# Kernel optimization log

Hardware: AMD Instinct MI355X
Metric: run time of the kernel (lower is better)

Reference implementation:

```python
import jax, jax.numpy as jnp
import numpy as np

B, S, D, UNITS = 8, 2048, 1024, 1024

def setup_inputs() -> dict:
    key = jax.random.key(0)
    k1, k2, k3, k4 = jax.random.split(key, 4)
    scale = 1.0 / np.sqrt(D)
    return {
        "inputs": jax.random.normal(k1, (B, S, D), dtype=jnp.float32),
        "Wq": jax.random.normal(k2, (D, UNITS), dtype=jnp.float32) * scale,
        "Wk": jax.random.normal(k3, (D, UNITS), dtype=jnp.float32) * scale,
        "Wv": jax.random.normal(k4, (D, UNITS), dtype=jnp.float32) * scale,
    }

def reference(inputs, Wq, Wk, Wv):
    # QKV projections (bias-free Dense): [B,S,D] @ [D,U] -> [B,S,U]
    q = jnp.einsum("bsd,du->bsu", inputs, Wq)
    k = jnp.einsum("bsd,du->bsu", inputs, Wk)
    v = jnp.einsum("bsd,du->bsu", inputs, Wv)
    # scaled dot-product scores [B,S,S]
    scores = jnp.einsum("bqu,bku->bqk", q, k) / jnp.sqrt(jnp.float32(UNITS))
    attn = jax.nn.softmax(scores, axis=-1)
    # weighted sum of values [B,S,U]
    return jnp.einsum("bqk,bku->bqu", attn, v)
```

## Files before the change

kernel.cpp:

```cpp
#include <hip/hip_runtime.h>


#define BM 128
#define BN 128
#define BK 64

typedef _Float16 half8  __attribute__((ext_vector_type(8)));
typedef float    floatx4 __attribute__((ext_vector_type(4)));

__device__ __forceinline__ void stage_async(const _Float16* __restrict__ src, int ld,
                                            _Float16* __restrict__ dst, int wave, int lane) {
#pragma unroll
    for (int i = 0; i < 4; ++i) {
        int chunk = i * 4 + wave;
        int L = chunk * 64 + lane;
        int row = L >> 3, c8 = L & 7;
        int cg = c8 ^ (row & 7);
        __builtin_amdgcn_global_load_lds(
            (const __attribute__((address_space(1))) unsigned int*)(src + (size_t)row * ld + cg * 8),
            (__attribute__((address_space(3))) unsigned int*)(dst + chunk * 512),
            16, 0, 0);
    }
}

__device__ __forceinline__ void mfma_accum(const _Float16* __restrict__ As,
                                           const _Float16* __restrict__ Bs,
                                           int wm, int wn, int l15, int q4,
                                           floatx4 acc[4][4]) {
#pragma unroll
    for (int kk = 0; kk < 2; ++kk) {
        half8 a[4], b[4];
#pragma unroll
        for (int i = 0; i < 4; ++i) {
            int row = wm * 64 + i * 16 + l15;
            int cg = (kk * 4 + q4) ^ (row & 7);
            a[i] = *(const half8*)(As + row * 64 + cg * 8);
        }
#pragma unroll
        for (int j = 0; j < 4; ++j) {
            int row = wn * 64 + j * 16 + l15;
            int cg = (kk * 4 + q4) ^ (row & 7);
            b[j] = *(const half8*)(Bs + row * 64 + cg * 8);
        }
#pragma unroll
        for (int i = 0; i < 4; ++i)
#pragma unroll
            for (int j = 0; j < 4; ++j)
                acc[i][j] = __builtin_amdgcn_mfma_f32_16x16x32_f16(a[i], b[j], acc[i][j], 0, 0, 0);
    }
}

__global__ void cast_x(const float* __restrict__ X, _Float16* __restrict__ Xh) {
    size_t i = ((size_t)blockIdx.x * 256 + threadIdx.x) * 8;
    float4 v0 = *(const float4*)(X + i);
    float4 v1 = *(const float4*)(X + i + 4);
    half8 h;
    h[0] = (_Float16)v0.x; h[1] = (_Float16)v0.y; h[2] = (_Float16)v0.z; h[3] = (_Float16)v0.w;
    h[4] = (_Float16)v1.x; h[5] = (_Float16)v1.y; h[6] = (_Float16)v1.z; h[7] = (_Float16)v1.w;
    *(half8*)(Xh + i) = h;
}

__global__ void prep_weights(const float* __restrict__ Wq, const float* __restrict__ Wk,
                             const float* __restrict__ Wv, _Float16* __restrict__ WbT,
                             float* __restrict__ rowsum) {
    int g = blockIdx.z;
    const float* W = (g == 0) ? Wq : (g == 1) ? Wk : Wv;
    __shared__ float tile[32][33];
    int u0 = blockIdx.x * 32, d0 = blockIdx.y * 32;
    int tx = threadIdx.x & 31, ty = threadIdx.x >> 5;
#pragma unroll
    for (int i = 0; i < 32; i += 8)
        tile[ty + i][tx] = W[(size_t)(d0 + ty + i) * 1024 + (u0 + tx)];
    __syncthreads();
#pragma unroll
    for (int i = 0; i < 32; i += 8)
        WbT[(size_t)g * 1024 * 1024 + (size_t)(u0 + ty + i) * 1024 + (d0 + tx)] =
            (_Float16)tile[tx][ty + i];
    int gid = (blockIdx.z * gridDim.y + blockIdx.y) * gridDim.x + blockIdx.x;
    int tg = gid * 256 + threadIdx.x;
    if (tg < 8 * 2048) rowsum[tg] = 0.0f;
}

__global__ void qkv_gemm(const _Float16* __restrict__ Xh, const _Float16* __restrict__ WbT,
                         _Float16* __restrict__ Qh, _Float16* __restrict__ Kh,
                         _Float16* __restrict__ Vt) {
    __shared__ __align__(16) _Float16 As[BM * BK];
    __shared__ __align__(16) _Float16 Bs[BN * BK];
    int t = threadIdx.x;
    int lane = t & 63, wave = t >> 6;
    int wm = wave >> 1, wn = wave & 1;
    int l15 = lane & 15, q4 = lane >> 4;
    int m0 = blockIdx.y * BM, n0 = blockIdx.x * BN;
    floatx4 acc[4][4] = {};
    for (int kt = 0; kt < 1024; kt += BK) {
        __syncthreads();
        stage_async(Xh + (size_t)m0 * 1024 + kt, 1024, As, wave, lane);
        stage_async(WbT + (size_t)n0 * 1024 + kt, 1024, Bs, wave, lane);
        __syncthreads();
        mfma_accum(As, Bs, wm, wn, l15, q4, acc);
    }
#pragma unroll
    for (int i = 0; i < 4; ++i)
#pragma unroll
        for (int j = 0; j < 4; ++j)
#pragma unroll
            for (int r = 0; r < 4; ++r) {
                int m = m0 + wm * 64 + i * 16 + q4 * 4 + r;
                int n = n0 + wn * 64 + j * 16 + l15;
                int which = n >> 10, u = n & 1023;
                int b = m >> 11, s = m & 2047;
                _Float16 val = (_Float16)acc[i][j][r];
                if (which == 0)      Qh[((size_t)b * 2048 + s) * 1024 + u] = val;
                else if (which == 1) Kh[((size_t)b * 2048 + s) * 1024 + u] = val;
                else                 Vt[((size_t)b * 1024 + u) * 2048 + s] = val;
            }
}

__global__ void scores_gemm(const _Float16* __restrict__ Qh, const _Float16* __restrict__ Kh,
                            _Float16* __restrict__ P, float* __restrict__ rowsum) {
    __shared__ __align__(16) _Float16 As[BM * BK];
    __shared__ __align__(16) _Float16 Bs[BN * BK];
    int t = threadIdx.x;
    int lane = t & 63, wave = t >> 6;
    int wm = wave >> 1, wn = wave & 1;
    int l15 = lane & 15, q4 = lane >> 4;
    int m0 = blockIdx.y * BM, n0 = blockIdx.x * BN;
    int batch = blockIdx.z;
    const _Float16* A = Qh + (size_t)batch * 2048 * 1024;
    const _Float16* B = Kh + (size_t)batch * 2048 * 1024;
    floatx4 acc[4][4] = {};
    for (int kt = 0; kt < 1024; kt += BK) {
        __syncthreads();
        stage_async(A + (size_t)m0 * 1024 + kt, 1024, As, wave, lane);
        stage_async(B + (size_t)n0 * 1024 + kt, 1024, Bs, wave, lane);
        __syncthreads();
        mfma_accum(As, Bs, wm, wn, l15, q4, acc);
    }
    _Float16* Pb = P + (size_t)batch * 2048 * 2048;
    float* rs = rowsum + batch * 2048;
#pragma unroll
    for (int i = 0; i < 4; ++i)
#pragma unroll
        for (int r = 0; r < 4; ++r) {
            int m = m0 + wm * 64 + i * 16 + q4 * 4 + r;
            float sum = 0.0f;
#pragma unroll
            for (int j = 0; j < 4; ++j) {
                int n = n0 + wn * 64 + j * 16 + l15;
                float e = __expf(acc[i][j][r] * 0.03125f);
                Pb[(size_t)m * 2048 + n] = (_Float16)e;
                sum += e;
            }
            sum += __shfl_xor(sum, 1);
            sum += __shfl_xor(sum, 2);
            sum += __shfl_xor(sum, 4);
            sum += __shfl_xor(sum, 8);
            if (l15 == 0) atomicAdd(&rs[m], sum);
        }
}

__global__ void pv_gemm(const _Float16* __restrict__ P, const _Float16* __restrict__ Vt,
                        const float* __restrict__ rowsum, float* __restrict__ out) {
    __shared__ __align__(16) _Float16 As[BM * BK];
    __shared__ __align__(16) _Float16 Bs[BN * BK];
    int t = threadIdx.x;
    int lane = t & 63, wave = t >> 6;
    int wm = wave >> 1, wn = wave & 1;
    int l15 = lane & 15, q4 = lane >> 4;
    int m0 = blockIdx.y * BM, n0 = blockIdx.x * BN;
    int batch = blockIdx.z;
    const _Float16* A = P + (size_t)batch * 2048 * 2048;
    const _Float16* B = Vt + (size_t)batch * 1024 * 2048;
    floatx4 acc[4][4] = {};
    for (int kt = 0; kt < 2048; kt += BK) {
        __syncthreads();
        stage_async(A + (size_t)m0 * 2048 + kt, 2048, As, wave, lane);
        stage_async(B + (size_t)n0 * 2048 + kt, 2048, Bs, wave, lane);
        __syncthreads();
        mfma_accum(As, Bs, wm, wn, l15, q4, acc);
    }
    const float* rs = rowsum + batch * 2048;
    float* ob = out + (size_t)batch * 2048 * 1024;
#pragma unroll
    for (int i = 0; i < 4; ++i)
#pragma unroll
        for (int r = 0; r < 4; ++r) {
            int m = m0 + wm * 64 + i * 16 + q4 * 4 + r;
            float inv = 1.0f / rs[m];
#pragma unroll
            for (int j = 0; j < 4; ++j) {
                int n = n0 + wn * 64 + j * 16 + l15;
                ob[(size_t)m * 1024 + n] = acc[i][j][r] * inv;
            }
        }
}

extern "C" void kernel_launch(void* const* d_in, const int* in_sizes, int n_in,
                              void* d_out, int out_size, void* d_ws, size_t ws_size,
                              hipStream_t stream) {
    const float* X  = (const float*)d_in[0];
    const float* Wq = (const float*)d_in[1];
    const float* Wk = (const float*)d_in[2];
    const float* Wv = (const float*)d_in[3];
    float* out = (float*)d_out;

    char* ws = (char*)d_ws;
    size_t off = 0;
    _Float16* Xh  = (_Float16*)(ws + off); off += (size_t)8 * 2048 * 1024 * 2;
    _Float16* WbT = (_Float16*)(ws + off); off += (size_t)3 * 1024 * 1024 * 2;
    _Float16* Qh  = (_Float16*)(ws + off); off += (size_t)8 * 2048 * 1024 * 2;
    _Float16* Kh  = (_Float16*)(ws + off); off += (size_t)8 * 2048 * 1024 * 2;
    _Float16* Vt  = (_Float16*)(ws + off); off += (size_t)8 * 1024 * 2048 * 2;
    _Float16* P   = (_Float16*)(ws + off); off += (size_t)8 * 2048 * 2048 * 2;
    float* rowsum = (float*)(ws + off);    off += (size_t)8 * 2048 * 4;

    cast_x     <<<dim3(8192, 1, 1), 256, 0, stream>>>(X, Xh);
    prep_weights<<<dim3(32, 32, 3), 256, 0, stream>>>(Wq, Wk, Wv, WbT, rowsum);
    qkv_gemm   <<<dim3(24, 128, 1), 256, 0, stream>>>(Xh, WbT, Qh, Kh, Vt);
    scores_gemm<<<dim3(16, 16, 8),  256, 0, stream>>>(Qh, Kh, P, rowsum);
    pv_gemm    <<<dim3(8, 16, 8),   256, 0, stream>>>(P, Vt, rowsum, out);
}
```

Baseline: 428.9 us.

## Switch to 32x32x16 MFMA and compute softmax row sums inside PV GEMM

Replaces the 16x16x32 MFMA tiling with 32x32x16 MFMA fragments in all three GEMMs, halving LDS fragment loads per FLOP. Removes the atomic row-sum accumulation from the scores epilogue and the zero-init in weight prep. Instead, pv_gemm sums the fp16 P values it already loads from LDS and normalizes with a lane shuffle. This trades global atomics for extra fp16 adds in the PV inner loop, and the sums now come from fp16-rounded P with half-precision partial adds, which may slightly change accuracy.

```diff
diff --git a/kernel.cpp b/kernel.cpp
--- a/kernel.cpp
+++ b/kernel.cpp
@@ -5,8 +5,9 @@
 #define BN 128
 #define BK 64
 
-typedef _Float16 half8  __attribute__((ext_vector_type(8)));
-typedef float    floatx4 __attribute__((ext_vector_type(4)));
+typedef _Float16 half8   __attribute__((ext_vector_type(8)));
+typedef _Float16 half2v  __attribute__((ext_vector_type(2)));
+typedef float    floatx16 __attribute__((ext_vector_type(16)));
 
 __device__ __forceinline__ void stage_async(const _Float16* __restrict__ src, int ld,
                                             _Float16* __restrict__ dst, int wave, int lane) {
@@ -25,44 +26,50 @@
 
 __device__ __forceinline__ void mfma_accum(const _Float16* __restrict__ As,
                                            const _Float16* __restrict__ Bs,
-                                           int wm, int wn, int l15, int q4,
-                                           floatx4 acc[4][4]) {
-#pragma unroll
-    for (int kk = 0; kk < 2; ++kk) {
-        half8 a[4], b[4];
-#pragma unroll
-        for (int i = 0; i < 4; ++i) {
-            int row = wm * 64 + i * 16 + l15;
-            int cg = (kk * 4 + q4) ^ (row & 7);
-            a[i] = *(const half8*)(As + row * 64 + cg * 8);
-        }
-#pragma unroll
-        for (int j = 0; j < 4; ++j) {
-            int row = wn * 64 + j * 16 + l15;
-            int cg = (kk * 4 + q4) ^ (row & 7);
-            b[j] = *(const half8*)(Bs + row * 64 + cg * 8);
-        }
-#pragma unroll
-        for (int i = 0; i < 4; ++i)
-#pragma unroll
-            for (int j = 0; j < 4; ++j)
-                acc[i][j] = __builtin_amdgcn_mfma_f32_16x16x32_f16(a[i], b[j], acc[i][j], 0, 0, 0);
-    }
+                                           int wm, int wn, int l31, int h,
+                                           floatx16 acc[2][2]) {
+#pragma unroll
+    for (int kc = 0; kc < 4; ++kc) {
+        int kh = kc * 2 + h;
+        half8 a[2], b[2];
+#pragma unroll
+        for (int fi = 0; fi < 2; ++fi) {
+            int row = wm * 64 + fi * 32 + l31;
+            a[fi] = *(const half8*)(As + row * 64 + (kh ^ (row & 7)) * 8);
+        }
+#pragma unroll
+        for (int fj = 0; fj < 2; ++fj) {
+            int row = wn * 64 + fj * 32 + l31;
+            b[fj] = *(const half8*)(Bs + row * 64 + (kh ^ (row & 7)) * 8);
+        }
+#pragma unroll
+        for (int fi = 0; fi < 2; ++fi)
+#pragma unroll
+            for (int fj = 0; fj < 2; ++fj)
+                acc[fi][fj] = __builtin_amdgcn_mfma_f32_32x32x16_f16(a[fi], b[fj], acc[fi][fj], 0, 0, 0);
+    }
+}
+
+__device__ __forceinline__ float sum8h(half8 a) {
+    union { half8 v; half2v h2[4]; } u; u.v = a;
+    half2v s0 = u.h2[0] + u.h2[1];
+    half2v s1 = u.h2[2] + u.h2[3];
+    half2v s  = s0 + s1;
+    return (float)s[0] + (float)s[1];
 }
 
 __global__ void cast_x(const float* __restrict__ X, _Float16* __restrict__ Xh) {
     size_t i = ((size_t)blockIdx.x * 256 + threadIdx.x) * 8;
     float4 v0 = *(const float4*)(X + i);
     float4 v1 = *(const float4*)(X + i + 4);
-    half8 h;
-    h[0] = (_Float16)v0.x; h[1] = (_Float16)v0.y; h[2] = (_Float16)v0.z; h[3] = (_Float16)v0.w;
-    h[4] = (_Float16)v1.x; h[5] = (_Float16)v1.y; h[6] = (_Float16)v1.z; h[7] = (_Float16)v1.w;
-    *(half8*)(Xh + i) = h;
+    half8 hh;
+    hh[0] = (_Float16)v0.x; hh[1] = (_Float16)v0.y; hh[2] = (_Float16)v0.z; hh[3] = (_Float16)v0.w;
+    hh[4] = (_Float16)v1.x; hh[5] = (_Float16)v1.y; hh[6] = (_Float16)v1.z; hh[7] = (_Float16)v1.w;
+    *(half8*)(Xh + i) = hh;
 }
 
 __global__ void prep_weights(const float* __restrict__ Wq, const float* __restrict__ Wk,
-                             const float* __restrict__ Wv, _Float16* __restrict__ WbT,
-                             float* __restrict__ rowsum) {
+                             const float* __restrict__ Wv, _Float16* __restrict__ WbT) {
     int g = blockIdx.z;
     const float* W = (g == 0) ? Wq : (g == 1) ? Wk : Wv;
     __shared__ float tile[32][33];
@@ -76,9 +83,6 @@
     for (int i = 0; i < 32; i += 8)
         WbT[(size_t)g * 1024 * 1024 + (size_t)(u0 + ty + i) * 1024 + (d0 + tx)] =
             (_Float16)tile[tx][ty + i];
-    int gid = (blockIdx.z * gridDim.y + blockIdx.y) * gridDim.x + blockIdx.x;
-    int tg = gid * 256 + threadIdx.x;
-    if (tg < 8 * 2048) rowsum[tg] = 0.0f;
 }
 
 __global__ void qkv_gemm(const _Float16* __restrict__ Xh, const _Float16* __restrict__ WbT,
@@ -89,27 +93,27 @@
     int t = threadIdx.x;
     int lane = t & 63, wave = t >> 6;
     int wm = wave >> 1, wn = wave & 1;
-    int l15 = lane & 15, q4 = lane >> 4;
+    int l31 = lane & 31, h = lane >> 5;
     int m0 = blockIdx.y * BM, n0 = blockIdx.x * BN;
-    floatx4 acc[4][4] = {};
+    floatx16 acc[2][2] = {};
     for (int kt = 0; kt < 1024; kt += BK) {
         __syncthreads();
         stage_async(Xh + (size_t)m0 * 1024 + kt, 1024, As, wave, lane);
         stage_async(WbT + (size_t)n0 * 1024 + kt, 1024, Bs, wave, lane);
         __syncthreads();
-        mfma_accum(As, Bs, wm, wn, l15, q4, acc);
-    }
-#pragma unroll
-    for (int i = 0; i < 4; ++i)
-#pragma unroll
-        for (int j = 0; j < 4; ++j)
-#pragma unroll
-            for (int r = 0; r < 4; ++r) {
-                int m = m0 + wm * 64 + i * 16 + q4 * 4 + r;
-                int n = n0 + wn * 64 + j * 16 + l15;
+        mfma_accum(As, Bs, wm, wn, l31, h, acc);
+    }
+#pragma unroll
+    for (int fi = 0; fi < 2; ++fi)
+#pragma unroll
+        for (int fj = 0; fj < 2; ++fj)
+#pragma unroll
+            for (int r = 0; r < 16; ++r) {
+                int m = m0 + wm * 64 + fi * 32 + (r & 3) + 8 * (r >> 2) + 4 * h;
+                int n = n0 + wn * 64 + fj * 32 + l31;
                 int which = n >> 10, u = n & 1023;
                 int b = m >> 11, s = m & 2047;
-                _Float16 val = (_Float16)acc[i][j][r];
+                _Float16 val = (_Float16)acc[fi][fj][r];
                 if (which == 0)      Qh[((size_t)b * 2048 + s) * 1024 + u] = val;
                 else if (which == 1) Kh[((size_t)b * 2048 + s) * 1024 + u] = val;
                 else                 Vt[((size_t)b * 1024 + u) * 2048 + s] = val;
@@ -117,80 +121,95 @@
 }
 
 __global__ void scores_gemm(const _Float16* __restrict__ Qh, const _Float16* __restrict__ Kh,
-                            _Float16* __restrict__ P, float* __restrict__ rowsum) {
+                            _Float16* __restrict__ P) {
     __shared__ __align__(16) _Float16 As[BM * BK];
     __shared__ __align__(16) _Float16 Bs[BN * BK];
     int t = threadIdx.x;
     int lane = t & 63, wave = t >> 6;
     int wm = wave >> 1, wn = wave & 1;
-    int l15 = lane & 15, q4 = lane >> 4;
+    int l31 = lane & 31, h = lane >> 5;
     int m0 = blockIdx.y * BM, n0 = blockIdx.x * BN;
     int batch = blockIdx.z;
     const _Float16* A = Qh + (size_t)batch * 2048 * 1024;
     const _Float16* B = Kh + (size_t)batch * 2048 * 1024;
-    floatx4 acc[4][4] = {};
+    floatx16 acc[2][2] = {};
     for (int kt = 0; kt < 1024; kt += BK) {
         __syncthreads();
         stage_async(A + (size_t)m0 * 1024 + kt, 1024, As, wave, lane);
         stage_async(B + (size_t)n0 * 1024 + kt, 1024, Bs, wave, lane);
         __syncthreads();
-        mfma_accum(As, Bs, wm, wn, l15, q4, acc);
+        mfma_accum(As, Bs, wm, wn, l31, h, acc);
     }
     _Float16* Pb = P + (size_t)batch * 2048 * 2048;
-    float* rs = rowsum + batch * 2048;
-#pragma unroll
-    for (int i = 0; i < 4; ++i)
-#pragma unroll
-        for (int r = 0; r < 4; ++r) {
-            int m = m0 + wm * 64 + i * 16 + q4 * 4 + r;
-            float sum = 0.0f;
-#pragma unroll
-            for (int j = 0; j < 4; ++j) {
-                int n = n0 + wn * 64 + j * 16 + l15;
-                float e = __expf(acc[i][j][r] * 0.03125f);
-                Pb[(size_t)m * 2048 + n] = (_Float16)e;
-                sum += e;
-            }
-            sum += __shfl_xor(sum, 1);
-            sum += __shfl_xor(sum, 2);
-            sum += __shfl_xor(sum, 4);
-            sum += __shfl_xor(sum, 8);
-            if (l15 == 0) atomicAdd(&rs[m], sum);
-        }
+#pragma unroll
+    for (int fi = 0; fi < 2; ++fi)
+#pragma unroll
+        for (int fj = 0; fj < 2; ++fj)
+#pragma unroll
+            for (int r = 0; r < 16; ++r) {
+                int m = m0 + wm * 64 + fi * 32 + (r & 3) + 8 * (r >> 2) + 4 * h;
+                int n = n0 + wn * 64 + fj * 32 + l31;
+                Pb[(size_t)m * 2048 + n] = (_Float16)__expf(acc[fi][fj][r] * 0.03125f);
+            }
 }
 
 __global__ void pv_gemm(const _Float16* __restrict__ P, const _Float16* __restrict__ Vt,
-                        const float* __restrict__ rowsum, float* __restrict__ out) {
+                        float* __restrict__ out) {
     __shared__ __align__(16) _Float16 As[BM * BK];
     __shared__ __align__(16) _Float16 Bs[BN * BK];
     int t = threadIdx.x;
     int lane = t & 63, wave = t >> 6;
     int wm = wave >> 1, wn = wave & 1;
-    int l15 = lane & 15, q4 = lane >> 4;
+    int l31 = lane & 31, h = lane >> 5;
     int m0 = blockIdx.y * BM, n0 = blockIdx.x * BN;
     int batch = blockIdx.z;
     const _Float16* A = P + (size_t)batch * 2048 * 2048;
     const _Float16* B = Vt + (size_t)batch * 1024 * 2048;
-    floatx4 acc[4][4] = {};
+    floatx16 acc[2][2] = {};
+    float rsum[2] = {0.0f, 0.0f};
     for (int kt = 0; kt < 2048; kt += BK) {
         __syncthreads();
         stage_async(A + (size_t)m0 * 2048 + kt, 2048, As, wave, lane);
         stage_async(B + (size_t)n0 * 2048 + kt, 2048, Bs, wave, lane);
         __syncthreads();
-        mfma_accum(As, Bs, wm, wn, l15, q4, acc);
-    }
-    const float* rs = rowsum + batch * 2048;
+#pragma unroll
+        for (int kc = 0; kc < 4; ++kc) {
+            int kh = kc * 2 + h;
+            half8 a[2], b[2];
+#pragma unroll
+            for (int fi = 0; fi < 2; ++fi) {
+                int row = wm * 64 + fi * 32 + l31;
+                a[fi] = *(const half8*)(As + row * 64 + (kh ^ (row & 7)) * 8);
+                rsum[fi] += sum8h(a[fi]);
+            }
+#pragma unroll
+            for (int fj = 0; fj < 2; ++fj) {
+                int row = wn * 64 + fj * 32 + l31;
+                b[fj] = *(const half8*)(Bs + row * 64 + (kh ^ (row & 7)) * 8);
+            }
+#pragma unroll
+            for (int fi = 0; fi < 2; ++fi)
+#pragma unroll
+                for (int fj = 0; fj < 2; ++fj)
+                    acc[fi][fj] = __builtin_amdgcn_mfma_f32_32x32x16_f16(a[fi], b[fj], acc[fi][fj], 0, 0, 0);
+        }
+    }
+    float rsumf[2];
+#pragma unroll
+    for (int fi = 0; fi < 2; ++fi)
+        rsumf[fi] = rsum[fi] + __shfl_xor(rsum[fi], 32);
     float* ob = out + (size_t)batch * 2048 * 1024;
 #pragma unroll
-    for (int i = 0; i < 4; ++i)
-#pragma unroll
-        for (int r = 0; r < 4; ++r) {
-            int m = m0 + wm * 64 + i * 16 + q4 * 4 + r;
-            float inv = 1.0f / rs[m];
-#pragma unroll
-            for (int j = 0; j < 4; ++j) {
-                int n = n0 + wn * 64 + j * 16 + l15;
-                ob[(size_t)m * 1024 + n] = acc[i][j][r] * inv;
+    for (int fi = 0; fi < 2; ++fi)
+#pragma unroll
+        for (int r = 0; r < 16; ++r) {
+            int row32 = (r & 3) + 8 * (r >> 2) + 4 * h;
+            float inv = 1.0f / __shfl(rsumf[fi], row32);
+            int m = m0 + wm * 64 + fi * 32 + row32;
+#pragma unroll
+            for (int fj = 0; fj < 2; ++fj) {
+                int n = n0 + wn * 64 + fj * 32 + l31;
+                ob[(size_t)m * 1024 + n] = acc[fi][fj][r] * inv;
             }
         }
 }
@@ -212,11 +231,10 @@
     _Float16* Kh  = (_Float16*)(ws + off); off += (size_t)8 * 2048 * 1024 * 2;
     _Float16* Vt  = (_Float16*)(ws + off); off += (size_t)8 * 1024 * 2048 * 2;
     _Float16* P   = (_Float16*)(ws + off); off += (size_t)8 * 2048 * 2048 * 2;
-    float* rowsum = (float*)(ws + off);    off += (size_t)8 * 2048 * 4;
-
-    cast_x     <<<dim3(8192, 1, 1), 256, 0, stream>>>(X, Xh);
-    prep_weights<<<dim3(32, 32, 3), 256, 0, stream>>>(Wq, Wk, Wv, WbT, rowsum);
-    qkv_gemm   <<<dim3(24, 128, 1), 256, 0, stream>>>(Xh, WbT, Qh, Kh, Vt);
-    scores_gemm<<<dim3(16, 16, 8),  256, 0, stream>>>(Qh, Kh, P, rowsum);
-    pv_gemm    <<<dim3(8, 16, 8),   256, 0, stream>>>(P, Vt, rowsum, out);
-}
+
+    cast_x      <<<dim3(8192, 1, 1), 256, 0, stream>>>(X, Xh);
+    prep_weights<<<dim3(32, 32, 3), 256, 0, stream>>>(Wq, Wk, Wv, WbT);
+    qkv_gemm    <<<dim3(24, 128, 1), 256, 0, stream>>>(Xh, WbT, Qh, Kh, Vt);
+    scores_gemm <<<dim3(16, 16, 8),  256, 0, stream>>>(Qh, Kh, P);
+    pv_gemm     <<<dim3(8, 16, 8),   256, 0, stream>>>(P, Vt, out);
+}
```

Result: slower. 492.4 us (+14.8%).

## Compute softmax row sums in PV GEMM and vectorize V-transpose stores

Applied to the files above, without the earlier changes.

The softmax denominator is no longer accumulated with atomics in the scores epilogue. Each PV GEMM block now sums the fp16 P values it already loads from LDS and reduces those partial sums with shuffles. Separately, the QKV epilogue picks the Q/K/V destination once per block and writes the transposed V as packed 4-half vectors instead of scalar strided stores. This removes the atomics, the rowsum buffer and its zeroing, at the cost of extra packed-half adds in the PV inner loop and some fp16 accumulation error in the row sums.

```diff
diff --git a/kernel.cpp b/kernel.cpp
--- a/kernel.cpp
+++ b/kernel.cpp
@@ -6,6 +6,8 @@
 #define BK 64
 
 typedef _Float16 half8  __attribute__((ext_vector_type(8)));
+typedef _Float16 half4v __attribute__((ext_vector_type(4)));
+typedef _Float16 half2v __attribute__((ext_vector_type(2)));
 typedef float    floatx4 __attribute__((ext_vector_type(4)));
 
 __device__ __forceinline__ void stage_async(const _Float16* __restrict__ src, int ld,
@@ -50,19 +52,26 @@
     }
 }
 
+__device__ __forceinline__ float sum8h(half8 a) {
+    union { half8 v; half2v h2[4]; } u; u.v = a;
+    half2v s0 = u.h2[0] + u.h2[1];
+    half2v s1 = u.h2[2] + u.h2[3];
+    half2v s  = s0 + s1;
+    return (float)s[0] + (float)s[1];
+}
+
 __global__ void cast_x(const float* __restrict__ X, _Float16* __restrict__ Xh) {
     size_t i = ((size_t)blockIdx.x * 256 + threadIdx.x) * 8;
     float4 v0 = *(const float4*)(X + i);
     float4 v1 = *(const float4*)(X + i + 4);
-    half8 h;
-    h[0] = (_Float16)v0.x; h[1] = (_Float16)v0.y; h[2] = (_Float16)v0.z; h[3] = (_Float16)v0.w;
-    h[4] = (_Float16)v1.x; h[5] = (_Float16)v1.y; h[6] = (_Float16)v1.z; h[7] = (_Float16)v1.w;
-    *(half8*)(Xh + i) = h;
+    half8 hh;
+    hh[0] = (_Float16)v0.x; hh[1] = (_Float16)v0.y; hh[2] = (_Float16)v0.z; hh[3] = (_Float16)v0.w;
+    hh[4] = (_Float16)v1.x; hh[5] = (_Float16)v1.y; hh[6] = (_Float16)v1.z; hh[7] = (_Float16)v1.w;
+    *(half8*)(Xh + i) = hh;
 }
 
 __global__ void prep_weights(const float* __restrict__ Wq, const float* __restrict__ Wk,
-                             const float* __restrict__ Wv, _Float16* __restrict__ WbT,
-                             float* __restrict__ rowsum) {
+                             const float* __restrict__ Wv, _Float16* __restrict__ WbT) {
     int g = blockIdx.z;
     const float* W = (g == 0) ? Wq : (g == 1) ? Wk : Wv;
     __shared__ float tile[32][33];
@@ -76,9 +85,6 @@
     for (int i = 0; i < 32; i += 8)
         WbT[(size_t)g * 1024 * 1024 + (size_t)(u0 + ty + i) * 1024 + (d0 + tx)] =
             (_Float16)tile[tx][ty + i];
-    int gid = (blockIdx.z * gridDim.y + blockIdx.y) * gridDim.x + blockIdx.x;
-    int tg = gid * 256 + threadIdx.x;
-    if (tg < 8 * 2048) rowsum[tg] = 0.0f;
 }
 
 __global__ void qkv_gemm(const _Float16* __restrict__ Xh, const _Float16* __restrict__ WbT,
@@ -99,25 +105,41 @@
         __syncthreads();
         mfma_accum(As, Bs, wm, wn, l15, q4, acc);
     }
-#pragma unroll
-    for (int i = 0; i < 4; ++i)
-#pragma unroll
-        for (int j = 0; j < 4; ++j)
-#pragma unroll
-            for (int r = 0; r < 4; ++r) {
-                int m = m0 + wm * 64 + i * 16 + q4 * 4 + r;
-                int n = n0 + wn * 64 + j * 16 + l15;
-                int which = n >> 10, u = n & 1023;
-                int b = m >> 11, s = m & 2047;
-                _Float16 val = (_Float16)acc[i][j][r];
-                if (which == 0)      Qh[((size_t)b * 2048 + s) * 1024 + u] = val;
-                else if (which == 1) Kh[((size_t)b * 2048 + s) * 1024 + u] = val;
-                else                 Vt[((size_t)b * 1024 + u) * 2048 + s] = val;
-            }
+    int which = blockIdx.x >> 3;
+    int u0 = (blockIdx.x & 7) * BN;
+    int b = m0 >> 11;
+    int sbase = (m0 & 2047) + wm * 64;
+    if (which < 2) {
+        _Float16* dst = which ? Kh : Qh;
+        _Float16* db = dst + (size_t)b * 2048 * 1024;
+#pragma unroll
+        for (int i = 0; i < 4; ++i)
+#pragma unroll
+            for (int j = 0; j < 4; ++j)
+#pragma unroll
+                for (int r = 0; r < 4; ++r) {
+                    int s = sbase + i * 16 + q4 * 4 + r;
+                    int u = u0 + wn * 64 + j * 16 + l15;
+                    db[(size_t)s * 1024 + u] = (_Float16)acc[i][j][r];
+                }
+    } else {
+        _Float16* vb = Vt + (size_t)b * 1024 * 2048;
+#pragma unroll
+        for (int i = 0; i < 4; ++i)
+#pragma unroll
+            for (int j = 0; j < 4; ++j) {
+                int s = sbase + i * 16 + q4 * 4;
+                int u = u0 + wn * 64 + j * 16 + l15;
+                half4v pk;
+#pragma unroll
+                for (int r = 0; r < 4; ++r) pk[r] = (_Float16)acc[i][j][r];
+                *(half4v*)(vb + (size_t)u * 2048 + s) = pk;
+            }
+    }
 }
 
 __global__ void scores_gemm(const _Float16* __restrict__ Qh, const _Float16* __restrict__ Kh,
-                            _Float16* __restrict__ P, float* __restrict__ rowsum) {
+                            _Float16* __restrict__ P) {
     __shared__ __align__(16) _Float16 As[BM * BK];
     __shared__ __align__(16) _Float16 Bs[BN * BK];
     int t = threadIdx.x;
@@ -137,30 +159,20 @@
         mfma_accum(As, Bs, wm, wn, l15, q4, acc);
     }
     _Float16* Pb = P + (size_t)batch * 2048 * 2048;
-    float* rs = rowsum + batch * 2048;
 #pragma unroll
     for (int i = 0; i < 4; ++i)
 #pragma unroll
-        for (int r = 0; r < 4; ++r) {
-            int m = m0 + wm * 64 + i * 16 + q4 * 4 + r;
-            float sum = 0.0f;
-#pragma unroll
-            for (int j = 0; j < 4; ++j) {
+        for (int j = 0; j < 4; ++j)
+#pragma unroll
+            for (int r = 0; r < 4; ++r) {
+                int m = m0 + wm * 64 + i * 16 + q4 * 4 + r;
                 int n = n0 + wn * 64 + j * 16 + l15;
-                float e = __expf(acc[i][j][r] * 0.03125f);
-                Pb[(size_t)m * 2048 + n] = (_Float16)e;
-                sum += e;
-            }
-            sum += __shfl_xor(sum, 1);
-            sum += __shfl_xor(sum, 2);
-            sum += __shfl_xor(sum, 4);
-            sum += __shfl_xor(sum, 8);
-            if (l15 == 0) atomicAdd(&rs[m], sum);
-        }
+                Pb[(size_t)m * 2048 + n] = (_Float16)__expf(acc[i][j][r] * 0.03125f);
+            }
 }
 
 __global__ void pv_gemm(const _Float16* __restrict__ P, const _Float16* __restrict__ Vt,
-                        const float* __restrict__ rowsum, float* __restrict__ out) {
+                        float* __restrict__ out) {
     __shared__ __align__(16) _Float16 As[BM * BK];
     __shared__ __align__(16) _Float16 Bs[BN * BK];
     int t = threadIdx.x;
@@ -172,21 +184,49 @@
     const _Float16* A = P + (size_t)batch * 2048 * 2048;
     const _Float16* B = Vt + (size_t)batch * 1024 * 2048;
     floatx4 acc[4][4] = {};
+    float rsum[4] = {0.f, 0.f, 0.f, 0.f};
     for (int kt = 0; kt < 2048; kt += BK) {
         __syncthreads();
         stage_async(A + (size_t)m0 * 2048 + kt, 2048, As, wave, lane);
         stage_async(B + (size_t)n0 * 2048 + kt, 2048, Bs, wave, lane);
         __syncthreads();
-        mfma_accum(As, Bs, wm, wn, l15, q4, acc);
-    }
-    const float* rs = rowsum + batch * 2048;
+#pragma unroll
+        for (int kk = 0; kk < 2; ++kk) {
+            half8 a[4], b[4];
+#pragma unroll
+            for (int i = 0; i < 4; ++i) {
+                int row = wm * 64 + i * 16 + l15;
+                int cg = (kk * 4 + q4) ^ (row & 7);
+                a[i] = *(const half8*)(As + row * 64 + cg * 8);
+                rsum[i] += sum8h(a[i]);
+            }
+#pragma unroll
+            for (int j = 0; j < 4; ++j) {
+                int row = wn * 64 + j * 16 + l15;
+                int cg = (kk * 4 + q4) ^ (row & 7);
+                b[j] = *(const half8*)(Bs + row * 64 + cg * 8);
+            }
+#pragma unroll
+            for (int i = 0; i < 4; ++i)
+#pragma unroll
+                for (int j = 0; j < 4; ++j)
+                    acc[i][j] = __builtin_amdgcn_mfma_f32_16x16x32_f16(a[i], b[j], acc[i][j], 0, 0, 0);
+        }
+    }
+    float rsumf[4];
+#pragma unroll
+    for (int i = 0; i < 4; ++i) {
+        float v = rsum[i] + __shfl_xor(rsum[i], 16);
+        rsumf[i] = v + __shfl_xor(v, 32);
+    }
     float* ob = out + (size_t)batch * 2048 * 1024;
 #pragma unroll
     for (int i = 0; i < 4; ++i)
 #pragma unroll
         for (int r = 0; r < 4; ++r) {
-            int m = m0 + wm * 64 + i * 16 + q4 * 4 + r;
-            float inv = 1.0f / rs[m];
+            int rloc = q4 * 4 + r;
+            float inv = 1.0f / __shfl(rsumf[i], rloc);
+            int m = m0 + wm * 64 + i * 16 + rloc;
 #pragma unroll
             for (int j = 0; j < 4; ++j) {
                 int n = n0 + wn * 64 + j * 16 + l15;
@@ -212,11 +252,10 @@
     _Float16* Kh  = (_Float16*)(ws + off); off += (size_t)8 * 2048 * 1024 * 2;
     _Float16* Vt  = (_Float16*)(ws + off); off += (size_t)8 * 1024 * 2048 * 2;
     _Float16* P   = (_Float16*)(ws + off); off += (size_t)8 * 2048 * 2048 * 2;
-    float* rowsum = (float*)(ws + off);    off += (size_t)8 * 2048 * 4;
-
-    cast_x     <<<dim3(8192, 1, 1), 256, 0, stream>>>(X, Xh);
-    prep_weights<<<dim3(32, 32, 3), 256, 0, stream>>>(Wq, Wk, Wv, WbT, rowsum);
-    qkv_gemm   <<<dim3(24, 128, 1), 256, 0, stream>>>(Xh, WbT, Qh, Kh, Vt);
-    scores_gemm<<<dim3(16, 16, 8),  256, 0, stream>>>(Qh, Kh, P, rowsum);
-    pv_gemm    <<<dim3(8, 16, 8),   256, 0, stream>>>(P, Vt, rowsum, out);
-}
+
+    cast_x      <<<dim3(8192, 1, 1), 256, 0, stream>>>(X, Xh);
+    prep_weights<<<dim3(32, 32, 3), 256, 0, stream>>>(Wq, Wk, Wv, WbT);
+    qkv_gemm    <<<dim3(24, 128, 1), 256, 0, stream>>>(Xh, WbT, Qh, Kh, Vt);
+    scores_gemm <<<dim3(16, 16, 8),  256, 0, stream>>>(Qh, Kh, P);
+    pv_gemm     <<<dim3(8, 16, 8),   256, 0, stream>>>(P, Vt, out);
+}
```

Result: faster. 398.6 us (-7.1%).
